# Kernel tuning notes

Measured on AMD Instinct MI355X. Metric: run time of the kernel, lower is better.

The kernel has to match this reference:

```python
import jax, jax.numpy as jnp
import numpy as np

B, L, D, N = 4, 2048, 1024, 16


def setup_inputs() -> dict:
    key = jax.random.key(0)
    ks = jax.random.split(key, 12)
    s = 1.0 / np.sqrt(D)
    inp = {
        'x': jax.random.normal(ks[0], (B, L, D), jnp.float32),
        'ln_g': jnp.ones((D,), jnp.float32),
        'ln_b': jnp.zeros((D,), jnp.float32),
        'w1_w': jax.random.normal(ks[1], (D, D), jnp.float32) * s,
        'w1_b': jnp.zeros((D,), jnp.float32),
        'v1_w': jax.random.normal(ks[2], (D, D), jnp.float32) * s,
        'v1_b': jnp.zeros((D,), jnp.float32),
        'w2_w': jax.random.normal(ks[3], (D, D), jnp.float32) * s,
        'w2_b': jnp.zeros((D,), jnp.float32),
        'conv_w': jax.random.normal(ks[4], (D, 1, 3), jnp.float32) * (1.0 / np.sqrt(3.0)),
        'A_log': jnp.log(jnp.broadcast_to(jnp.arange(1, N + 1, dtype=jnp.float32), (D, N))),
        'D_skip': jnp.ones((D,), jnp.float32),
        'W_dt': jax.random.normal(ks[5], (D, D), jnp.float32) * (s * 0.1),
        'b_dt': jnp.full((D,), -4.0, jnp.float32),
        'W_B': jax.random.normal(ks[6], (D, N), jnp.float32) * s,
        'W_C': jax.random.normal(ks[7], (D, N), jnp.float32) * s,
    }
    return inp


def _layernorm(x, g, b, eps=1e-5):
    mu = jnp.mean(x, axis=-1, keepdims=True)
    var = jnp.mean(jnp.square(x - mu), axis=-1, keepdims=True)
    return (x - mu) * jax.lax.rsqrt(var + eps) * g + b


def _silu(x):
    return x * jax.nn.sigmoid(x)


def _depthwise_conv(x, w):
    # x: (B, L, D), w: (D, 1, 3), padding=1, groups=D
    xc = x.transpose(0, 2, 1)  # (B, D, L)
    y = jax.lax.conv_general_dilated(
        xc, w, window_strides=(1,), padding=[(1, 1)],
        feature_group_count=xc.shape[1],
        dimension_numbers=('NCH', 'OIH', 'NCH'))
    return y.transpose(0, 2, 1)


def _selective_scan(u, A_log, D_skip, W_dt, b_dt, W_B, W_C):
    # u: (B, L, D) -> y: (B, L, D); diagonal selective SSM (Mamba S6)
    A = -jnp.exp(A_log)                              # (D, N)
    dt = jax.nn.softplus(u @ W_dt + b_dt)            # (B, L, D)
    Bt = u @ W_B                                     # (B, L, N)
    Ct = u @ W_C                                     # (B, L, N)

    def step(h, inp):
        dt_t, B_t, C_t, u_t = inp                    # (B,D),(B,N),(B,N),(B,D)
        dA = jnp.exp(dt_t[..., None] * A)            # (B, D, N)
        h = dA * h + (dt_t * u_t)[..., None] * B_t[:, None, :]
        y = jnp.einsum('bdn,bn->bd', h, C_t)
        return h, y

    h0 = jnp.zeros((u.shape[0], u.shape[2], A.shape[1]), u.dtype)
    xs = (dt.transpose(1, 0, 2), Bt.transpose(1, 0, 2),
          Ct.transpose(1, 0, 2), u.transpose(1, 0, 2))
    _, ys = jax.lax.scan(step, h0, xs)               # ys: (L, B, D)
    return ys.transpose(1, 0, 2) + u * D_skip


def reference(x, ln_g, ln_b, w1_w, w1_b, v1_w, v1_b, w2_w, w2_b, conv_w,
              A_log, D_skip, W_dt, b_dt, W_B, W_C):
    x_norm = _layernorm(x, ln_g, ln_b)
    x1 = x_norm @ w1_w + w1_b
    x_conv = _silu(_depthwise_conv(x1, conv_w))
    x_ssm = _selective_scan(x_conv, A_log, D_skip, W_dt, b_dt, W_B, W_C)
    v = _silu(x_norm @ v1_w + v1_b)
    return (x_ssm * v) @ w2_w + w2_b
```

## Files before the change

kernel.cpp:

```cpp
#include <hip/hip_runtime.h>
#include <hip/hip_bf16.h>

#define BB 4
#define LL 2048
#define DD 1024
#define NN 16
#define BL (BB * LL)
#define NC 32
#define LC 64

typedef float f32x4 __attribute__((ext_vector_type(4)));
typedef __bf16 bf16x8 __attribute__((ext_vector_type(8)));

typedef __attribute__((address_space(1))) unsigned int as1_u32;
typedef __attribute__((address_space(3))) unsigned int as3_u32;

__device__ __forceinline__ void gl_lds16(const void* g, void* l) {
  __builtin_amdgcn_global_load_lds((as1_u32*)g, (as3_u32*)l, 16, 0, 0);
}

__device__ __forceinline__ float fast_sigmoid(float x) {
  return 1.f / (1.f + __expf(-x));
}

__global__ __launch_bounds__(256) void k_prep(const float* __restrict__ w1,
                                              const float* __restrict__ v1,
                                              const float* __restrict__ wdt,
                                              const float* __restrict__ w2,
                                              const float* __restrict__ WB,
                                              const float* __restrict__ WC,
                                              __hip_bfloat16* __restrict__ wcat,
                                              __hip_bfloat16* __restrict__ wdtbc,
                                              __hip_bfloat16* __restrict__ w2T) {
  const int z = blockIdx.z;
  if (z < 4) {
    const float* src = (z == 0) ? w1 : (z == 1) ? v1 : (z == 2) ? wdt : w2;
    __hip_bfloat16* dst = (z == 0) ? wcat
                        : (z == 1) ? (wcat + (size_t)1024 * DD)
                        : (z == 2) ? wdtbc : w2T;
    __shared__ float tile[32][33];
    const int kt = blockIdx.x * 32, nt = blockIdx.y * 32;
    const int tx = threadIdx.x & 31, ty = threadIdx.x >> 5;
#pragma unroll
    for (int j = 0; j < 32; j += 8)
      tile[ty + j][tx] = src[(size_t)(kt + ty + j) * DD + nt + tx];
    __syncthreads();
#pragma unroll
    for (int j = 0; j < 32; j += 8)
      dst[(size_t)(nt + ty + j) * DD + kt + tx] = __float2bfloat16(tile[tx][ty + j]);
  } else {
    const int id = blockIdx.y * 32 + blockIdx.x;
    if (id < 128) {
      const int idx = id * 256 + threadIdx.x;
      const int k = idx & 1023, n = idx >> 10;
      const float v = (n < 16) ? WB[(size_t)k * 16 + n] : WC[(size_t)k * 16 + (n - 16)];
      wdtbc[(size_t)(1024 + n) * DD + k] = __float2bfloat16(v);
    } else if (id < 512) {
      const int idx = (id - 128) * 256 + threadIdx.x;
      wdtbc[(size_t)1056 * DD + idx] = __float2bfloat16(0.f);
    }
  }
}

__global__ __launch_bounds__(256) void k_layernorm(const float* __restrict__ x,
                                                   const float* __restrict__ g,
                                                   const float* __restrict__ b,
                                                   __hip_bfloat16* __restrict__ out) {
  const int row = blockIdx.x;
  const int tid = threadIdx.x;
  const f32x4 xv = *(const f32x4*)(x + (size_t)row * DD + tid * 4);
  float s = xv[0] + xv[1] + xv[2] + xv[3];
  float sq = xv[0] * xv[0] + xv[1] * xv[1] + xv[2] * xv[2] + xv[3] * xv[3];
#pragma unroll
  for (int o = 32; o > 0; o >>= 1) {
    s += __shfl_down(s, o);
    sq += __shfl_down(sq, o);
  }
  __shared__ float red[8];
  const int wave = tid >> 6, lane = tid & 63;
  if (lane == 0) { red[wave] = s; red[4 + wave] = sq; }
  __syncthreads();
  s = red[0] + red[1] + red[2] + red[3];
  sq = red[4] + red[5] + red[6] + red[7];
  const float mean = s * (1.f / DD);
  const float var = sq * (1.f / DD) - mean * mean;
  const float rs = rsqrtf(var + 1e-5f);
  const f32x4 gv = *(const f32x4*)(g + tid * 4);
  const f32x4 bv = *(const f32x4*)(b + tid * 4);
  union { ushort4 u; __hip_bfloat16 h[4]; } cv;
#pragma unroll
  for (int j = 0; j < 4; ++j)
    cv.h[j] = __float2bfloat16((xv[j] - mean) * rs * gv[j] + bv[j]);
  *reinterpret_cast<ushort4*>(&out[(size_t)row * DD + tid * 4]) = cv.u;
}

template <int EPI>
__device__ __forceinline__ void gemm_body(const __hip_bfloat16* __restrict__ Ag,
                                          const __hip_bfloat16* __restrict__ Wg,
                                          void* __restrict__ o0, void* __restrict__ o1,
                                          void* __restrict__ o2,
                                          const float* __restrict__ bias0,
                                          const float* __restrict__ bias1) {
  __shared__ unsigned short As[2][128 * 32];
  __shared__ unsigned short Bs[2][128 * 32];
  const int tid = threadIdx.x;
  const int wave = tid >> 6, lane = tid & 63;
  const int quad = lane >> 4, l16 = lane & 15;
  const int wm = wave & 1, wn = wave >> 1;

  const int srow = wave * 32 + (lane >> 2);
  const int sbyte = (lane & 3) * 16;
  const char* gA = (const char*)(Ag + (size_t)(blockIdx.x * 128 + srow) * 1024) + sbyte;
  const char* gB = (const char*)(Wg + (size_t)(blockIdx.y * 128 + srow) * 1024) + sbyte;
  char* lA[2] = {(char*)&As[0][0] + wave * 2048, (char*)&As[1][0] + wave * 2048};
  char* lB[2] = {(char*)&Bs[0][0] + wave * 2048, (char*)&Bs[1][0] + wave * 2048};

  gl_lds16(gA, lA[0]);
  gl_lds16(gA + 16 * 2048, lA[0] + 1024);
  gl_lds16(gB, lB[0]);
  gl_lds16(gB + 16 * 2048, lB[0] + 1024);
  gA += 64;
  gB += 64;
  __syncthreads();

  f32x4 acc[4][4] = {};

  for (int kt = 0; kt < 32; ++kt) {
    const int cur = kt & 1, nxt = cur ^ 1;
    if (kt < 31) {
      gl_lds16(gA, lA[nxt]);
      gl_lds16(gA + 16 * 2048, lA[nxt] + 1024);
      gl_lds16(gB, lB[nxt]);
      gl_lds16(gB + 16 * 2048, lB[nxt] + 1024);
      gA += 64;
      gB += 64;
    }
    const unsigned short* Ab = &As[cur][0];
    const unsigned short* Bb = &Bs[cur][0];
    bf16x8 af[4], bfr[4];
#pragma unroll
    for (int i = 0; i < 4; ++i) {
      af[i] = *(const bf16x8*)(Ab + (wm * 64 + i * 16 + l16) * 32 + quad * 8);
      bfr[i] = *(const bf16x8*)(Bb + (wn * 64 + i * 16 + l16) * 32 + quad * 8);
    }
#pragma unroll
    for (int i = 0; i < 4; ++i)
#pragma unroll
      for (int j = 0; j < 4; ++j)
        acc[i][j] = __builtin_amdgcn_mfma_f32_16x16x32_bf16(af[i], bfr[j], acc[i][j], 0, 0, 0);
    __syncthreads();
  }

  const int m0 = blockIdx.x * 128 + wm * 64 + quad * 4;
  const int n0 = blockIdx.y * 128 + wn * 64 + l16;
#pragma unroll
  for (int i = 0; i < 4; ++i) {
#pragma unroll
    for (int r = 0; r < 4; ++r) {
      const int m = m0 + i * 16 + r;
#pragma unroll
      for (int j = 0; j < 4; ++j) {
        const int n = n0 + j * 16;
        const float val = acc[i][j][r];
        if constexpr (EPI == 1) {
          if (n < 1024) {
            ((__hip_bfloat16*)o0)[(size_t)m * DD + n] = __float2bfloat16(val + bias0[n]);
          } else {
            const float t = val + bias1[n - 1024];
            ((__hip_bfloat16*)o1)[(size_t)m * DD + (n - 1024)] =
                __float2bfloat16(t * fast_sigmoid(t));
          }
        } else if constexpr (EPI == 2) {
          if (n < 1024) {
            const float t = val + bias0[n];
            const float sp = (t > 15.f) ? t : __logf(1.f + __expf(t));
            ((__hip_bfloat16*)o0)[(size_t)m * DD + n] = __float2bfloat16(sp);
          } else if (n < 1040) {
            ((float*)o1)[(size_t)m * NN + (n - 1024)] = val;
          } else if (n < 1056) {
            ((float*)o2)[(size_t)m * NN + (n - 1040)] = val;
          }
        } else {
          ((float*)o0)[(size_t)m * DD + n] = val + bias0[n];
        }
      }
    }
  }
}

__global__ __launch_bounds__(256) void k_gemm_xv(const __hip_bfloat16* __restrict__ Ag,
                                                 const __hip_bfloat16* __restrict__ Wg,
                                                 void* o0, void* o1,
                                                 const float* __restrict__ b0,
                                                 const float* __restrict__ b1) {
  gemm_body<1>(Ag, Wg, o0, o1, nullptr, b0, b1);
}
__global__ __launch_bounds__(256) void k_gemm_dbc(const __hip_bfloat16* __restrict__ Ag,
                                                  const __hip_bfloat16* __restrict__ Wg,
                                                  void* o0, void* o1, void* o2,
                                                  const float* __restrict__ b0) {
  gemm_body<2>(Ag, Wg, o0, o1, o2, b0, nullptr);
}
__global__ __launch_bounds__(256) void k_gemm_out(const __hip_bfloat16* __restrict__ Ag,
                                                  const __hip_bfloat16* __restrict__ Wg,
                                                  void* o0, const float* __restrict__ b0) {
  gemm_body<3>(Ag, Wg, o0, nullptr, nullptr, b0, nullptr);
}

__global__ __launch_bounds__(256) void k_conv_silu(const __hip_bfloat16* __restrict__ x1,
                                                   const float* __restrict__ w,
                                                   __hip_bfloat16* __restrict__ out) {
  const size_t e = ((size_t)blockIdx.x * 256 + threadIdx.x) * 8;
  const int d = (int)(e & 1023);
  const int l = (int)((e >> 10) & 2047);
  const bf16x8 zero = {};
  const bf16x8 xm = (l > 0) ? *(const bf16x8*)(x1 + e - DD) : zero;
  const bf16x8 x0 = *(const bf16x8*)(x1 + e);
  const bf16x8 xp = (l < LL - 1) ? *(const bf16x8*)(x1 + e + DD) : zero;
  bf16x8 o;
#pragma unroll
  for (int j = 0; j < 8; ++j) {
    const float w0 = w[(d + j) * 3 + 0], w1 = w[(d + j) * 3 + 1], w2 = w[(d + j) * 3 + 2];
    const float a = w0 * (float)xm[j] + w1 * (float)x0[j] + w2 * (float)xp[j];
    o[j] = (__bf16)(a * fast_sigmoid(a));
  }
  *(bf16x8*)(out + e) = o;
}

__global__ __launch_bounds__(256) void k_scan1(const __hip_bfloat16* __restrict__ dt,
                                               const __hip_bfloat16* __restrict__ u,
                                               const float* __restrict__ Bt,
                                               const float* __restrict__ A_log,
                                               float* __restrict__ P,
                                               float* __restrict__ hend) {
  const int d = blockIdx.x * 256 + threadIdx.x;
  const int c = blockIdx.y, b = blockIdx.z;
  __shared__ float Bsh[LC * NN];
  ((f32x4*)Bsh)[threadIdx.x] = ((const f32x4*)(Bt + (size_t)(b * LL + c * LC) * NN))[threadIdx.x];
  float a[NN];
#pragma unroll
  for (int n = 0; n < NN; ++n) a[n] = -__expf(A_log[(size_t)d * NN + n]);
  __syncthreads();
  float h[NN] = {};
  float sdt = 0.f;
  size_t idx = (size_t)(b * LL + c * LC) * DD + d;
#pragma unroll 4
  for (int t = 0; t < LC; ++t, idx += DD) {
    const float dtv = __bfloat162float(dt[idx]);
    const float uv = __bfloat162float(u[idx]);
    sdt += dtv;
    const float du = dtv * uv;
#pragma unroll
    for (int n = 0; n < NN; ++n)
      h[n] = __expf(dtv * a[n]) * h[n] + du * Bsh[t * NN + n];
  }
  const size_t o = ((size_t)((b * NC + c) * DD + d)) * NN;
#pragma unroll
  for (int n = 0; n < NN; ++n) {
    P[o + n] = __expf(sdt * a[n]);
    hend[o + n] = h[n];
  }
}

__global__ __launch_bounds__(256) void k_scan2(const float* __restrict__ P, float* __restrict__ h) {
  const int gidx = blockIdx.x * 256 + threadIdx.x;
  const int n = gidx & 15, d = (gidx >> 4) & 1023, b = gidx >> 14;
  float hs = 0.f;
  size_t off = ((size_t)b * NC * DD + d) * NN + n;
  const size_t stride = (size_t)DD * NN;
  for (int c = 0; c < NC; ++c, off += stride) {
    const float he = h[off];
    const float p = P[off];
    h[off] = hs;
    hs = p * hs + he;
  }
}

__global__ __launch_bounds__(256) void k_scan3(const __hip_bfloat16* __restrict__ dt,
                                               const __hip_bfloat16* __restrict__ u,
                                               const float* __restrict__ Bt,
                                               const float* __restrict__ Ct,
                                               const float* __restrict__ A_log,
                                               const float* __restrict__ hstart,
                                               const float* __restrict__ Dskip,
                                               const __hip_bfloat16* __restrict__ v,
                                               __hip_bfloat16* __restrict__ yA) {
  const int d = blockIdx.x * 256 + threadIdx.x;
  const int c = blockIdx.y, b = blockIdx.z;
  __shared__ float Bsh[LC * NN];
  __shared__ float Csh[LC * NN];
  ((f32x4*)Bsh)[threadIdx.x] = ((const f32x4*)(Bt + (size_t)(b * LL + c * LC) * NN))[threadIdx.x];
  ((f32x4*)Csh)[threadIdx.x] = ((const f32x4*)(Ct + (size_t)(b * LL + c * LC) * NN))[threadIdx.x];
  float a[NN];
#pragma unroll
  for (int n = 0; n < NN; ++n) a[n] = -__expf(A_log[(size_t)d * NN + n]);
  const float dsk = Dskip[d];
  float h[NN];
  const size_t o = ((size_t)((b * NC + c) * DD + d)) * NN;
#pragma unroll
  for (int n = 0; n < NN; ++n) h[n] = hstart[o + n];
  __syncthreads();
  size_t idx = (size_t)(b * LL + c * LC) * DD + d;
#pragma unroll 2
  for (int t = 0; t < LC; ++t, idx += DD) {
    const float dtv = __bfloat162float(dt[idx]);
    const float uv = __bfloat162float(u[idx]);
    const float du = dtv * uv;
    float y = 0.f;
#pragma unroll
    for (int n = 0; n < NN; ++n) {
      h[n] = __expf(dtv * a[n]) * h[n] + du * Bsh[t * NN + n];
      y += h[n] * Csh[t * NN + n];
    }
    const float xssm = y + uv * dsk;
    const float vv = __bfloat162float(v[idx]);
    yA[idx] = __float2bfloat16(xssm * vv);
  }
}

extern "C" void kernel_launch(void* const* d_in, const int* in_sizes, int n_in,
                              void* d_out, int out_size, void* d_ws, size_t ws_size,
                              hipStream_t stream) {
  const float* x      = (const float*)d_in[0];
  const float* ln_g   = (const float*)d_in[1];
  const float* ln_b   = (const float*)d_in[2];
  const float* w1_w   = (const float*)d_in[3];
  const float* w1_b   = (const float*)d_in[4];
  const float* v1_w   = (const float*)d_in[5];
  const float* v1_b   = (const float*)d_in[6];
  const float* w2_w   = (const float*)d_in[7];
  const float* w2_b   = (const float*)d_in[8];
  const float* conv_w = (const float*)d_in[9];
  const float* A_log  = (const float*)d_in[10];
  const float* D_skip = (const float*)d_in[11];
  const float* W_dt   = (const float*)d_in[12];
  const float* b_dt   = (const float*)d_in[13];
  const float* W_B    = (const float*)d_in[14];
  const float* W_C    = (const float*)d_in[15];

  char* ws = (char*)d_ws;
  const size_t OFF_SLOTA = 0;
  const size_t OFF_SLOTB = 16777216;
  const size_t OFF_VBUF  = 33554432;
  const size_t OFF_YA    = 50331648;
  const size_t OFF_WCAT  = 67108864;
  const size_t OFF_WDTBC = 71303168;
  const size_t OFF_W2T   = 73662464;
  const size_t OFF_BT    = 75759616;
  const size_t OFF_CT    = 76283904;
  const size_t OFF_P     = 76808192;
  const size_t OFF_H     = 85196800;

  __hip_bfloat16* xnorm = (__hip_bfloat16*)(ws + OFF_SLOTA);
  __hip_bfloat16* xconv = (__hip_bfloat16*)(ws + OFF_SLOTA);
  __hip_bfloat16* x1    = (__hip_bfloat16*)(ws + OFF_SLOTB);
  __hip_bfloat16* dtb   = (__hip_bfloat16*)(ws + OFF_SLOTB);
  __hip_bfloat16* vbuf  = (__hip_bfloat16*)(ws + OFF_VBUF);
  __hip_bfloat16* yA    = (__hip_bfloat16*)(ws + OFF_YA);
  __hip_bfloat16* wcat  = (__hip_bfloat16*)(ws + OFF_WCAT);
  __hip_bfloat16* wdtbc = (__hip_bfloat16*)(ws + OFF_WDTBC);
  __hip_bfloat16* w2T   = (__hip_bfloat16*)(ws + OFF_W2T);
  float* Btf = (float*)(ws + OFF_BT);
  float* Ctf = (float*)(ws + OFF_CT);
  float* P   = (float*)(ws + OFF_P);
  float* H   = (float*)(ws + OFF_H);

  k_prep<<<dim3(32, 32, 5), 256, 0, stream>>>(w1_w, v1_w, W_dt, w2_w, W_B, W_C,
                                              wcat, wdtbc, w2T);

  k_layernorm<<<BL, 256, 0, stream>>>(x, ln_g, ln_b, xnorm);

  k_gemm_xv<<<dim3(BL / 128, 2048 / 128), 256, 0, stream>>>(
      xnorm, wcat, (void*)x1, (void*)vbuf, w1_b, v1_b);

  k_conv_silu<<<(BL * DD / 8) / 256, 256, 0, stream>>>(x1, conv_w, xconv);

  k_gemm_dbc<<<dim3(BL / 128, 1152 / 128), 256, 0, stream>>>(
      xconv, wdtbc, (void*)dtb, (void*)Btf, (void*)Ctf, b_dt);

  k_scan1<<<dim3(DD / 256, NC, BB), 256, 0, stream>>>(dtb, xconv, Btf, A_log, P, H);
  k_scan2<<<(BB * DD * NN) / 256, 256, 0, stream>>>(P, H);
  k_scan3<<<dim3(DD / 256, NC, BB), 256, 0, stream>>>(dtb, xconv, Btf, Ctf, A_log, H, D_skip,
                                                      vbuf, yA);

  k_gemm_out<<<dim3(BL / 128, 1024 / 128), 256, 0, stream>>>(yA, w2T, d_out, w2_b);
}
```

Measured before the change: 375.3 us.

## Load GEMM fragments directly from global into registers, bypassing LDS staging

The shared GEMM body stops staging A/B tiles in LDS through global_load_lds with double buffering and barriers. Each wave now loads its MFMA fragments straight from global memory into registers, double-buffered in registers across the K loop. This removes LDS traffic and __syncthreads. In exchange, tiles are no longer shared between waves, so global and L1/L2 traffic roughly doubles, and loads are less coalesced. The final prefetch also reads past the last K chunk.

```diff
diff --git a/kernel.cpp b/kernel.cpp
--- a/kernel.cpp
+++ b/kernel.cpp
@@ -11,13 +11,6 @@
 
 typedef float f32x4 __attribute__((ext_vector_type(4)));
 typedef __bf16 bf16x8 __attribute__((ext_vector_type(8)));
-
-typedef __attribute__((address_space(1))) unsigned int as1_u32;
-typedef __attribute__((address_space(3))) unsigned int as3_u32;
-
-__device__ __forceinline__ void gl_lds16(const void* g, void* l) {
-  __builtin_amdgcn_global_load_lds((as1_u32*)g, (as3_u32*)l, 16, 0, 0);
-}
 
 __device__ __forceinline__ float fast_sigmoid(float x) {
   return 1.f / (1.f + __expf(-x));
@@ -101,66 +94,60 @@
                                           void* __restrict__ o2,
                                           const float* __restrict__ bias0,
                                           const float* __restrict__ bias1) {
-  __shared__ unsigned short As[2][128 * 32];
-  __shared__ unsigned short Bs[2][128 * 32];
   const int tid = threadIdx.x;
   const int wave = tid >> 6, lane = tid & 63;
   const int quad = lane >> 4, l16 = lane & 15;
   const int wm = wave & 1, wn = wave >> 1;
-
-  const int srow = wave * 32 + (lane >> 2);
-  const int sbyte = (lane & 3) * 16;
-  const char* gA = (const char*)(Ag + (size_t)(blockIdx.x * 128 + srow) * 1024) + sbyte;
-  const char* gB = (const char*)(Wg + (size_t)(blockIdx.y * 128 + srow) * 1024) + sbyte;
-  char* lA[2] = {(char*)&As[0][0] + wave * 2048, (char*)&As[1][0] + wave * 2048};
-  char* lB[2] = {(char*)&Bs[0][0] + wave * 2048, (char*)&Bs[1][0] + wave * 2048};
-
-  gl_lds16(gA, lA[0]);
-  gl_lds16(gA + 16 * 2048, lA[0] + 1024);
-  gl_lds16(gB, lB[0]);
-  gl_lds16(gB + 16 * 2048, lB[0] + 1024);
-  gA += 64;
-  gB += 64;
-  __syncthreads();
+  const int m0 = blockIdx.x * 128 + wm * 64;
+  const int n0 = blockIdx.y * 128 + wn * 64;
+  const __hip_bfloat16* ap = Ag + (size_t)(m0 + l16) * 1024 + quad * 8;
+  const __hip_bfloat16* bp = Wg + (size_t)(n0 + l16) * 1024 + quad * 8;
+  constexpr size_t RS = (size_t)16 * 1024;
 
   f32x4 acc[4][4] = {};
-
-  for (int kt = 0; kt < 32; ++kt) {
-    const int cur = kt & 1, nxt = cur ^ 1;
-    if (kt < 31) {
-      gl_lds16(gA, lA[nxt]);
-      gl_lds16(gA + 16 * 2048, lA[nxt] + 1024);
-      gl_lds16(gB, lB[nxt]);
-      gl_lds16(gB + 16 * 2048, lB[nxt] + 1024);
-      gA += 64;
-      gB += 64;
-    }
-    const unsigned short* Ab = &As[cur][0];
-    const unsigned short* Bb = &Bs[cur][0];
-    bf16x8 af[4], bfr[4];
+  bf16x8 a0[4], b0[4], a1[4], b1[4];
+
+#pragma unroll
+  for (int i = 0; i < 4; ++i) {
+    a0[i] = *(const bf16x8*)(ap + i * RS);
+    b0[i] = *(const bf16x8*)(bp + i * RS);
+  }
+
+  for (int kt = 0; kt < 16; ++kt) {
+    const __hip_bfloat16* apk = ap + (2 * kt + 1) * 32;
+    const __hip_bfloat16* bpk = bp + (2 * kt + 1) * 32;
 #pragma unroll
     for (int i = 0; i < 4; ++i) {
-      af[i] = *(const bf16x8*)(Ab + (wm * 64 + i * 16 + l16) * 32 + quad * 8);
-      bfr[i] = *(const bf16x8*)(Bb + (wn * 64 + i * 16 + l16) * 32 + quad * 8);
+      a1[i] = *(const bf16x8*)(apk + i * RS);
+      b1[i] = *(const bf16x8*)(bpk + i * RS);
     }
 #pragma unroll
     for (int i = 0; i < 4; ++i)
 #pragma unroll
       for (int j = 0; j < 4; ++j)
-        acc[i][j] = __builtin_amdgcn_mfma_f32_16x16x32_bf16(af[i], bfr[j], acc[i][j], 0, 0, 0);
-    __syncthreads();
-  }
-
-  const int m0 = blockIdx.x * 128 + wm * 64 + quad * 4;
-  const int n0 = blockIdx.y * 128 + wn * 64 + l16;
+        acc[i][j] = __builtin_amdgcn_mfma_f32_16x16x32_bf16(a0[i], b0[j], acc[i][j], 0, 0, 0);
+#pragma unroll
+    for (int i = 0; i < 4; ++i) {
+      a0[i] = *(const bf16x8*)(apk + 32 + i * RS);
+      b0[i] = *(const bf16x8*)(bpk + 32 + i * RS);
+    }
+#pragma unroll
+    for (int i = 0; i < 4; ++i)
+#pragma unroll
+      for (int j = 0; j < 4; ++j)
+        acc[i][j] = __builtin_amdgcn_mfma_f32_16x16x32_bf16(a1[i], b1[j], acc[i][j], 0, 0, 0);
+  }
+
+  const int em0 = blockIdx.x * 128 + wm * 64 + quad * 4;
+  const int en0 = blockIdx.y * 128 + wn * 64 + l16;
 #pragma unroll
   for (int i = 0; i < 4; ++i) {
 #pragma unroll
     for (int r = 0; r < 4; ++r) {
-      const int m = m0 + i * 16 + r;
+      const int m = em0 + i * 16 + r;
 #pragma unroll
       for (int j = 0; j < 4; ++j) {
-        const int n = n0 + j * 16;
+        const int n = en0 + j * 16;
         const float val = acc[i][j][r];
         if constexpr (EPI == 1) {
           if (n < 1024) {
```

Result: slower. 556.8 us (+48.3%).
